# Optimization experiments

Measured on AMD Instinct MI355X. Metric: run time of the kernel, lower is better.

The kernel has to match this reference:

```python
import jax, jax.numpy as jnp
import numpy as np

NUM_CODES = 8192
EMBED_DIM = 512


def setup_inputs() -> dict:
    key = jax.random.key(0)
    k1, k2 = jax.random.split(key)
    inputs = jax.random.normal(k1, (8, 2048, EMBED_DIM), dtype=jnp.float32)
    # torch init: uniform(-1/num_codes, 1/num_codes)
    codebook = jax.random.uniform(
        k2, (NUM_CODES, EMBED_DIM), dtype=jnp.float32,
        minval=-1.0 / NUM_CODES, maxval=1.0 / NUM_CODES)
    return {"inputs": inputs, "codebook": codebook}


def reference(inputs, codebook):
    sg = jax.lax.stop_gradient
    D = codebook.shape[1]
    flat = inputs.reshape(-1, D)                      # [N, D]
    dist = (jnp.sum(flat * flat, axis=1, keepdims=True)
            + jnp.sum(codebook * codebook, axis=1)
            - 2.0 * jnp.matmul(flat, codebook.T))
    encoding_indices = jnp.argmin(dist, axis=1)       # [N]
    quantized = codebook[encoding_indices].reshape(inputs.shape)
    q_latent_loss = jnp.mean((quantized - sg(inputs)) ** 2)
    e_latent_loss = jnp.mean((sg(quantized) - inputs) ** 2)
    quantized_out = inputs + sg(quantized - inputs)   # straight-through
    idx = encoding_indices.reshape(inputs.shape[:-1])
    return (quantized_out, q_latent_loss, e_latent_loss, quantized, idx)
```

## Files before the change

### kernel.cpp

```cpp
#include <hip/hip_runtime.h>

typedef unsigned long long u64;
typedef unsigned int u32;
typedef unsigned short u16;
typedef unsigned char u8;

#define N_ROWS 16384
#define DIM    512
#define K_CODES 8192

#define CHUNKS 64
#define CHUNK_CODES 128
#define BMR 128
#define KC 64
#define KTILES (DIM / KC)

typedef int   i32x4  __attribute__((ext_vector_type(4)));
typedef int   i32x8  __attribute__((ext_vector_type(8)));
typedef float f32x16 __attribute__((ext_vector_type(16)));

__device__ __forceinline__ void t3_insert(u64* a, u64 k) {
    u64 x = k;
    bool l0 = x < a[0]; u64 n0 = l0 ? x : a[0]; x = l0 ? a[0] : x;
    bool l1 = x < a[1]; u64 n1 = l1 ? x : a[1]; x = l1 ? a[1] : x;
    bool l2 = x < a[2]; u64 n2 = l2 ? x : a[2];
    a[0] = n0; a[1] = n1; a[2] = n2;
}

__global__ void vq_split_kernel(const float* __restrict__ x, const float* __restrict__ cb,
                                u32* __restrict__ xf8, u32* __restrict__ cf8) {
    size_t t = (size_t)blockIdx.x * blockDim.x + threadIdx.x;
    const size_t nx = (size_t)N_ROWS * DIM / 4;
    const size_t nc = (size_t)K_CODES * DIM / 4;
    if (t < nx) {
        float4 v = ((const float4*)x)[t];
        u32 r = (u32)__builtin_amdgcn_cvt_pk_fp8_f32(v.x, v.y, 0, false);
        r = (u32)__builtin_amdgcn_cvt_pk_fp8_f32(v.z, v.w, (int)r, true);
        xf8[t] = r;
    } else if (t < nx + nc) {
        float4 v = ((const float4*)cb)[t - nx];
        u32 r = (u32)__builtin_amdgcn_cvt_pk_fp8_f32(v.x * 8192.0f, v.y * 8192.0f, 0, false);
        r = (u32)__builtin_amdgcn_cvt_pk_fp8_f32(v.z * 8192.0f, v.w * 8192.0f, (int)r, true);
        cf8[t - nx] = r;
    }
}

__global__ void vq_np_norm_kernel(const float* __restrict__ x, const float* __restrict__ cb,
                                  float* __restrict__ Arow, float* __restrict__ Bcode) {
    int wid = (blockIdx.x * blockDim.x + threadIdx.x) >> 6;
    int lane = threadIdx.x & 63;
    int r2 = lane >> 5;
    int b  = (lane >> 3) & 3;
    int j  = lane & 7;
    int row = wid * 2 + r2;
    const float* p;
    float* o;
    if (row < N_ROWS) { p = x + (size_t)row * DIM; o = Arow + row; }
    else              { int c = row - N_ROWS; p = cb + (size_t)c * DIM; o = Bcode + c; }
    const float* q = p + b * 128 + j;
    float v0 = q[0];
    float s = __fmul_rn(v0, v0);
    #pragma unroll
    for (int i = 1; i < 16; ++i) {
        float v = q[8 * i];
        s = __fadd_rn(s, __fmul_rn(v, v));
    }
    s = __fadd_rn(s, __shfl_xor(s, 1));
    s = __fadd_rn(s, __shfl_xor(s, 2));
    s = __fadd_rn(s, __shfl_xor(s, 4));
    s = __fadd_rn(s, __shfl_xor(s, 8));
    s = __fadd_rn(s, __shfl_xor(s, 16));
    if ((lane & 31) == 0) *o = s;
}

__launch_bounds__(256, 3)
__global__ void vq_screen_kernel(const u8* __restrict__ xf8, const u8* __restrict__ cf8,
                                 u64* __restrict__ top3out) {
    __shared__ __align__(16) u8 lds[3][16384];

    const int t = threadIdx.x;
    const int lane = t & 63;
    const int w = t >> 6;
    const int wrow  = w >> 1;
    const int wcode = w & 1;
    const int l31 = lane & 31;
    const int h = lane >> 5;

    const int rowBase   = blockIdx.x * BMR;
    const int chunkBase = blockIdx.y * CHUNK_CODES;

    const size_t laneOff = (size_t)(lane >> 2) * DIM
                         + (size_t)(((lane & 3) ^ ((lane >> 3) & 3)) * 16);
    const u8* srcs[4];
    int dsts[4];
    #pragma unroll
    for (int j = 0; j < 4; ++j) {
        int q = j * 4 + w;
        const u8* gp = (q < 8) ? (xf8 + (size_t)(rowBase + q * 16) * DIM)
                               : (cf8 + (size_t)(chunkBase + (q - 8) * 16) * DIM);
        srcs[j] = gp + laneOff;
        dsts[j] = q * 1024;
    }

    auto stage = [&](int kt) {
        u8* B = &lds[kt % 3][0];
        #pragma unroll
        for (int j = 0; j < 4; ++j) {
            __builtin_amdgcn_global_load_lds(
                (const __attribute__((address_space(1))) u32*)(srcs[j] + kt * KC),
                (__attribute__((address_space(3))) u32*)(B + dsts[j]),
                16, 0, 0);
        }
    };

    const int swz = (l31 >> 1) & 3;
    const int s0 = ((h * 2 + 0) ^ swz) * 16;
    const int s1 = ((h * 2 + 1) ^ swz) * 16;
    int aOff0[2], aOff1[2], bOff0[2], bOff1[2];
    #pragma unroll
    for (int mi = 0; mi < 2; ++mi) {
        int rc = wcode * 64 + mi * 32 + l31;
        aOff0[mi] = 8192 + rc * 64 + s0;
        aOff1[mi] = 8192 + rc * 64 + s1;
    }
    #pragma unroll
    for (int ni = 0; ni < 2; ++ni) {
        int rx = wrow * 64 + ni * 32 + l31;
        bOff0[ni] = rx * 64 + s0;
        bOff1[ni] = rx * 64 + s1;
    }

    f32x16 acc[2][2] = {};

    stage(0);
    stage(1);

    #pragma unroll
    for (int kt = 0; kt < KTILES; ++kt) {
        if (kt + 1 < KTILES) {
            asm volatile("s_waitcnt vmcnt(4)" ::: "memory");
        } else {
            asm volatile("s_waitcnt vmcnt(0)" ::: "memory");
        }
        asm volatile("s_barrier" ::: "memory");
        if (kt + 2 < KTILES) stage(kt + 2);

        const u8* L = &lds[kt % 3][0];
        i32x8 Af[2], Bf[2];
        #pragma unroll
        for (int mi = 0; mi < 2; ++mi) {
            *(i32x4*)&Af[mi]       = *(const i32x4*)(L + aOff0[mi]);
            *((i32x4*)&Af[mi] + 1) = *(const i32x4*)(L + aOff1[mi]);
        }
        #pragma unroll
        for (int ni = 0; ni < 2; ++ni) {
            *(i32x4*)&Bf[ni]       = *(const i32x4*)(L + bOff0[ni]);
            *((i32x4*)&Bf[ni] + 1) = *(const i32x4*)(L + bOff1[ni]);
        }
        __builtin_amdgcn_s_setprio(1);
        #pragma unroll
        for (int ni = 0; ni < 2; ++ni)
            #pragma unroll
            for (int mi = 0; mi < 2; ++mi)
                acc[mi][ni] = __builtin_amdgcn_mfma_scale_f32_32x32x64_f8f6f4(
                    Af[mi], Bf[ni], acc[mi][ni], 0, 0, 0, 127, 0, 127);
        __builtin_amdgcn_s_setprio(0);
    }

    __syncthreads();
    u64* t3buf = (u64*)&lds[0][0];

    #pragma unroll
    for (int ni = 0; ni < 2; ++ni) {
        float v0 = -3.4e38f, v1 = -3.4e38f, v2 = -3.4e38f;
        int   i0 = 0, i1 = 0, i2 = 0;
        #pragma unroll
        for (int mi = 0; mi < 2; ++mi) {
            const int cb0 = chunkBase + wcode * 64 + mi * 32 + 4 * h;
            #pragma unroll
            for (int reg = 0; reg < 16; ++reg) {
                float v = acc[mi][ni][reg];
                int idx = cb0 + (reg & 3) + 8 * (reg >> 2);
                bool c0 = v > v0, c1 = v > v1, c2 = v > v2;
                v2 = c1 ? v1 : (c2 ? v : v2); i2 = c1 ? i1 : (c2 ? idx : i2);
                v1 = c0 ? v0 : (c1 ? v : v1); i1 = c0 ? i0 : (c1 ? idx : i1);
                v0 = c0 ? v  : v0;            i0 = c0 ? idx : i0;
            }
        }
        float w0 = __shfl_xor(v0, 32), w1 = __shfl_xor(v1, 32), w2 = __shfl_xor(v2, 32);
        int   j0 = __shfl_xor(i0, 32), j1 = __shfl_xor(i1, 32), j2 = __shfl_xor(i2, 32);
        #pragma unroll
        for (int s = 0; s < 3; ++s) {
            float ov = (s == 0) ? w0 : (s == 1) ? w1 : w2;
            int   oi = (s == 0) ? j0 : (s == 1) ? j1 : j2;
            bool c0 = ov > v0, c1 = ov > v1, c2 = ov > v2;
            v2 = c1 ? v1 : (c2 ? ov : v2); i2 = c1 ? i1 : (c2 ? oi : i2);
            v1 = c0 ? v0 : (c1 ? ov : v1); i1 = c0 ? i0 : (c1 ? oi : i1);
            v0 = c0 ? ov : v0;             i0 = c0 ? oi  : i0;
        }
        if (h == 0) {
            int xrl = wrow * 64 + ni * 32 + l31;
            u32 b0 = __float_as_uint(v0);
            u32 k0 = (v0 < 0.0f) ? b0 : (~b0 & 0x7FFFFFFFu);
            u32 b1 = __float_as_uint(v1);
            u32 k1 = (v1 < 0.0f) ? b1 : (~b1 & 0x7FFFFFFFu);
            u32 b2 = __float_as_uint(v2);
            u32 k2 = (v2 < 0.0f) ? b2 : (~b2 & 0x7FFFFFFFu);
            t3buf[(xrl * 2 + wcode) * 3 + 0] = ((u64)k0 << 13) | (u32)i0;
            t3buf[(xrl * 2 + wcode) * 3 + 1] = ((u64)k1 << 13) | (u32)i1;
            t3buf[(xrl * 2 + wcode) * 3 + 2] = ((u64)k2 << 13) | (u32)i2;
        }
    }
    __syncthreads();
    if (t < BMR) {
        u64 best[3];
        best[0] = t3buf[(t * 2 + 0) * 3 + 0];
        best[1] = t3buf[(t * 2 + 0) * 3 + 1];
        best[2] = t3buf[(t * 2 + 0) * 3 + 2];
        t3_insert(best, t3buf[(t * 2 + 1) * 3 + 0]);
        t3_insert(best, t3buf[(t * 2 + 1) * 3 + 1]);
        t3_insert(best, t3buf[(t * 2 + 1) * 3 + 2]);
        size_t o = ((size_t)blockIdx.y * N_ROWS + rowBase + t) * 3;
        top3out[o + 0] = best[0];
        top3out[o + 1] = best[1];
        top3out[o + 2] = best[2];
    }
}

__global__ void vq_refine_kernel(const float* __restrict__ x, const float* __restrict__ cb,
                                 const float* __restrict__ Arow, const float* __restrict__ Bcode,
                                 const u64* __restrict__ top3, int* __restrict__ idxOut,
                                 float* __restrict__ out4) {
    int gw = (blockIdx.x * blockDim.x + threadIdx.x) >> 6;
    int lane = threadIdx.x & 63;
    if (gw >= N_ROWS) return;

    const u64* tp = top3 + ((size_t)lane * N_ROWS + gw) * 3;
    u64 a0 = tp[0], a1 = tp[1], a2 = tp[2];

    u64 cand[8];
    #pragma unroll
    for (int j = 0; j < 8; ++j) {
        u64 m = a0;
        #pragma unroll
        for (int s = 1; s < 64; s <<= 1) { u64 o = __shfl_xor(m, s); m = o < m ? o : m; }
        cand[j] = m;
        if (a0 == m) { a0 = a1; a1 = a2; a2 = ~0ull; }
    }

    float Ai = Arow[gw];
    const float* xr = x + (size_t)gw * DIM;
    float xv[8];
    #pragma unroll
    for (int e = 0; e < 8; ++e) xv[e] = xr[e * 64 + lane];

    u64 best = ~0ull;
    #pragma unroll
    for (int j = 0; j < 8; ++j) {
        int c = (int)(cand[j] & 8191u);
        const float* er = cb + (size_t)c * DIM;
        double d = 0.0;
        #pragma unroll
        for (int e = 0; e < 8; ++e)
            d = fma((double)xv[e], (double)er[e * 64 + lane], d);
        #pragma unroll
        for (int m = 1; m < 64; m <<= 1) d += __shfl_xor(d, m);
        float m32 = (float)d;
        float dist = __fsub_rn(__fadd_rn(Ai, Bcode[c]), 2.0f * m32);
        u64 ek = ((u64)__float_as_uint(dist) << 13) | (u64)(u32)c;
        best = ek < best ? ek : best;
    }
    if (lane == 0) {
        int c = (int)(best & 8191u);
        idxOut[gw] = c;
        out4[gw] = (float)c;
    }
}

__global__ void vq_gather_kernel(const float* __restrict__ x,
                                 const float* __restrict__ cb,
                                 const int* __restrict__ idxArr,
                                 float* __restrict__ out0,
                                 float* __restrict__ out3,
                                 float* __restrict__ rowPart) {
    int gw = (blockIdx.x * blockDim.x + threadIdx.x) >> 6;
    int lane = threadIdx.x & 63;
    if (gw >= N_ROWS) return;
    int idx = idxArr[gw];
    const float2* xp = (const float2*)(x  + (size_t)gw * DIM);
    const float2* qp = (const float2*)(cb + (size_t)idx * DIM);
    float2* o0 = (float2*)(out0 + (size_t)gw * DIM);
    float2* o3 = (float2*)(out3 + (size_t)gw * DIM);
    float part = 0.0f;
    #pragma unroll
    for (int r = 0; r < 4; ++r) {
        int e = r * 64 + lane;
        float2 xv = xp[e];
        float2 qv = qp[e];
        float dx = qv.x - xv.x, dy = qv.y - xv.y;
        part += dx * dx + dy * dy;
        float2 o; o.x = xv.x + dx; o.y = xv.y + dy;
        o0[e] = o;
        o3[e] = qv;
    }
    #pragma unroll
    for (int m = 32; m; m >>= 1) part += __shfl_xor(part, m);
    if (lane == 0) rowPart[gw] = part;
}

__global__ void vq_loss_kernel(const float* __restrict__ rowPart,
                               float* __restrict__ out1, float* __restrict__ out2) {
    __shared__ float red[256];
    int t = threadIdx.x;
    float s = 0.0f;
    for (int r = t; r < N_ROWS; r += 256) s += rowPart[r];
    red[t] = s;
    __syncthreads();
    #pragma unroll
    for (int m = 128; m; m >>= 1) {
        if (t < m) red[t] += red[t + m];
        __syncthreads();
    }
    if (t == 0) {
        float loss = red[0] / (float)(N_ROWS * DIM);
        out1[0] = loss;
        out2[0] = loss;
    }
}

extern "C" void kernel_launch(void* const* d_in, const int* in_sizes, int n_in,
                              void* d_out, int out_size, void* d_ws, size_t ws_size,
                              hipStream_t stream) {
    const float* x  = (const float*)d_in[0];
    const float* cb = (const float*)d_in[1];
    float* out  = (float*)d_out;
    float* out0 = out;
    float* out1 = out + 8388608;
    float* out2 = out + 8388609;
    float* out3 = out + 8388610;
    float* out4 = out + 16777218;

    u32* xf8   = (u32*)out0;
    u32* cf8   = (u32*)(out + 2097152);
    u64* wsTop3 = (u64*)(out + 8388612);

    char* ws = (char*)d_ws;
    float* wsA    = (float*)ws;
    float* wsB    = (float*)(ws + 65536);
    int*   wsIdx  = (int*)(ws + 98304);
    float* wsPart = (float*)(ws + 163840);

    hipLaunchKernelGGL(vq_split_kernel,   dim3(12288), dim3(256), 0, stream,
                       x, cb, xf8, cf8);
    hipLaunchKernelGGL(vq_np_norm_kernel, dim3(3072), dim3(256), 0, stream, x, cb, wsA, wsB);
    hipLaunchKernelGGL(vq_screen_kernel,  dim3(N_ROWS / BMR, CHUNKS), dim3(256), 0, stream,
                       (const u8*)xf8, (const u8*)cf8, wsTop3);
    hipLaunchKernelGGL(vq_refine_kernel,  dim3(4096), dim3(256), 0, stream,
                       x, cb, wsA, wsB, wsTop3, wsIdx, out4);
    hipLaunchKernelGGL(vq_gather_kernel,  dim3(4096), dim3(256), 0, stream,
                       x, cb, wsIdx, out0, out3, wsPart);
    hipLaunchKernelGGL(vq_loss_kernel,    dim3(1),    dim3(256), 0, stream,
                       wsPart, out1, out2);
}
```

Measured before the change: 203.8 us.

## Reorganize LDS tile layout and pack code index into float mantissa for top-3

Changes the global-to-LDS staging so each lane loads one whole row and 16-byte K-slices are placed in separate 2KB slot planes. This replaces the XOR-swizzled row-major layout and aims at conflict-free fragment reads with simpler offsets. The top-3 selection now packs the 13-bit code index into the low mantissa bits of the dot-product float and uses fmax/fmin networks instead of compare-select on separate value/index pairs. That cuts VALU work and register use, but the global loads become less coalesced (per-lane stride of DIM). Truncating the mantissa also loses precision, which could change near-tie screening.

```diff
diff --git a/kernel.cpp b/kernel.cpp
--- a/kernel.cpp
+++ b/kernel.cpp
@@ -25,6 +25,13 @@
     bool l1 = x < a[1]; u64 n1 = l1 ? x : a[1]; x = l1 ? a[1] : x;
     bool l2 = x < a[2]; u64 n2 = l2 ? x : a[2];
     a[0] = n0; a[1] = n1; a[2] = n2;
+}
+
+__device__ __forceinline__ void f3_insert(float& v0, float& v1, float& v2, float p) {
+    float n0 = fmaxf(p, v0);
+    float n1 = fminf(fmaxf(p, v1), v0);
+    float n2 = fminf(fmaxf(p, v2), v1);
+    v0 = n0; v1 = n1; v2 = n2;
 }
 
 __global__ void vq_split_kernel(const float* __restrict__ x, const float* __restrict__ cb,
@@ -89,17 +96,17 @@
     const int rowBase   = blockIdx.x * BMR;
     const int chunkBase = blockIdx.y * CHUNK_CODES;
 
-    const size_t laneOff = (size_t)(lane >> 2) * DIM
-                         + (size_t)(((lane & 3) ^ ((lane >> 3) & 3)) * 16);
     const u8* srcs[4];
     int dsts[4];
     #pragma unroll
     for (int j = 0; j < 4; ++j) {
         int q = j * 4 + w;
-        const u8* gp = (q < 8) ? (xf8 + (size_t)(rowBase + q * 16) * DIM)
-                               : (cf8 + (size_t)(chunkBase + (q - 8) * 16) * DIM);
-        srcs[j] = gp + laneOff;
-        dsts[j] = q * 1024;
+        int qq = q & 7;
+        int slot = qq & 3, rh = qq >> 2;
+        const u8* gp = (q < 8) ? (xf8 + (size_t)(rowBase + rh * 64 + lane) * DIM)
+                               : (cf8 + (size_t)(chunkBase + rh * 64 + lane) * DIM);
+        srcs[j] = gp + slot * 16;
+        dsts[j] = (q < 8 ? 0 : 8192) + slot * 2048 + rh * 1024;
     }
 
     auto stage = [&](int kt) {
@@ -113,21 +120,18 @@
         }
     };
 
-    const int swz = (l31 >> 1) & 3;
-    const int s0 = ((h * 2 + 0) ^ swz) * 16;
-    const int s1 = ((h * 2 + 1) ^ swz) * 16;
     int aOff0[2], aOff1[2], bOff0[2], bOff1[2];
     #pragma unroll
     for (int mi = 0; mi < 2; ++mi) {
         int rc = wcode * 64 + mi * 32 + l31;
-        aOff0[mi] = 8192 + rc * 64 + s0;
-        aOff1[mi] = 8192 + rc * 64 + s1;
+        aOff0[mi] = 8192 + (h * 2 + 0) * 2048 + rc * 16;
+        aOff1[mi] = 8192 + (h * 2 + 1) * 2048 + rc * 16;
     }
     #pragma unroll
     for (int ni = 0; ni < 2; ++ni) {
         int rx = wrow * 64 + ni * 32 + l31;
-        bOff0[ni] = rx * 64 + s0;
-        bOff1[ni] = rx * 64 + s1;
+        bOff0[ni] = (h * 2 + 0) * 2048 + rx * 16;
+        bOff1[ni] = (h * 2 + 1) * 2048 + rx * 16;
     }
 
     f32x16 acc[2][2] = {};
@@ -172,43 +176,32 @@
 
     #pragma unroll
     for (int ni = 0; ni < 2; ++ni) {
-        float v0 = -3.4e38f, v1 = -3.4e38f, v2 = -3.4e38f;
-        int   i0 = 0, i1 = 0, i2 = 0;
+        float p0 = -3.4e38f, p1 = -3.4e38f, p2 = -3.4e38f;
         #pragma unroll
         for (int mi = 0; mi < 2; ++mi) {
-            const int cb0 = chunkBase + wcode * 64 + mi * 32 + 4 * h;
+            const u32 cb0u = (u32)(chunkBase + wcode * 64 + mi * 32 + 4 * h);
             #pragma unroll
             for (int reg = 0; reg < 16; ++reg) {
-                float v = acc[mi][ni][reg];
-                int idx = cb0 + (reg & 3) + 8 * (reg >> 2);
-                bool c0 = v > v0, c1 = v > v1, c2 = v > v2;
-                v2 = c1 ? v1 : (c2 ? v : v2); i2 = c1 ? i1 : (c2 ? idx : i2);
-                v1 = c0 ? v0 : (c1 ? v : v1); i1 = c0 ? i0 : (c1 ? idx : i1);
-                v0 = c0 ? v  : v0;            i0 = c0 ? idx : i0;
+                u32 pr = (__float_as_uint(acc[mi][ni][reg]) & 0xFFFFE000u)
+                       | cb0u | (u32)((reg & 3) + 8 * (reg >> 2));
+                f3_insert(p0, p1, p2, __uint_as_float(pr));
             }
         }
-        float w0 = __shfl_xor(v0, 32), w1 = __shfl_xor(v1, 32), w2 = __shfl_xor(v2, 32);
-        int   j0 = __shfl_xor(i0, 32), j1 = __shfl_xor(i1, 32), j2 = __shfl_xor(i2, 32);
-        #pragma unroll
-        for (int s = 0; s < 3; ++s) {
-            float ov = (s == 0) ? w0 : (s == 1) ? w1 : w2;
-            int   oi = (s == 0) ? j0 : (s == 1) ? j1 : j2;
-            bool c0 = ov > v0, c1 = ov > v1, c2 = ov > v2;
-            v2 = c1 ? v1 : (c2 ? ov : v2); i2 = c1 ? i1 : (c2 ? oi : i2);
-            v1 = c0 ? v0 : (c1 ? ov : v1); i1 = c0 ? i0 : (c1 ? oi : i1);
-            v0 = c0 ? ov : v0;             i0 = c0 ? oi  : i0;
-        }
+        float q0 = __shfl_xor(p0, 32), q1 = __shfl_xor(p1, 32), q2 = __shfl_xor(p2, 32);
+        f3_insert(p0, p1, p2, q0);
+        f3_insert(p0, p1, p2, q1);
+        f3_insert(p0, p1, p2, q2);
         if (h == 0) {
             int xrl = wrow * 64 + ni * 32 + l31;
-            u32 b0 = __float_as_uint(v0);
-            u32 k0 = (v0 < 0.0f) ? b0 : (~b0 & 0x7FFFFFFFu);
-            u32 b1 = __float_as_uint(v1);
-            u32 k1 = (v1 < 0.0f) ? b1 : (~b1 & 0x7FFFFFFFu);
-            u32 b2 = __float_as_uint(v2);
-            u32 k2 = (v2 < 0.0f) ? b2 : (~b2 & 0x7FFFFFFFu);
-            t3buf[(xrl * 2 + wcode) * 3 + 0] = ((u64)k0 << 13) | (u32)i0;
-            t3buf[(xrl * 2 + wcode) * 3 + 1] = ((u64)k1 << 13) | (u32)i1;
-            t3buf[(xrl * 2 + wcode) * 3 + 2] = ((u64)k2 << 13) | (u32)i2;
+            u32 s0 = __float_as_uint(p0);
+            u32 k0 = (p0 < 0.0f) ? s0 : (~s0 & 0x7FFFFFFFu);
+            u32 s1 = __float_as_uint(p1);
+            u32 k1 = (p1 < 0.0f) ? s1 : (~s1 & 0x7FFFFFFFu);
+            u32 s2 = __float_as_uint(p2);
+            u32 k2 = (p2 < 0.0f) ? s2 : (~s2 & 0x7FFFFFFFu);
+            t3buf[(xrl * 2 + wcode) * 3 + 0] = ((u64)k0 << 13) | (u64)(s0 & 8191u);
+            t3buf[(xrl * 2 + wcode) * 3 + 1] = ((u64)k1 << 13) | (u64)(s1 & 8191u);
+            t3buf[(xrl * 2 + wcode) * 3 + 2] = ((u64)k2 << 13) | (u64)(s2 & 8191u);
         }
     }
     __syncthreads();
```

Measured after the change: 229.7 us. 1.13x slower.
